# Kernel tuning notes

Hardware: AMD Instinct MI355X
Metric: run time of the kernel (lower is better)

Reference implementation:

```python
import jax, jax.numpy as jnp
import numpy as np
import math

B, CIN, COUT, NSC, H, W = 4, 3, 64, 3, 192, 192
HID = 64  # attention hidden channels


def setup_inputs() -> dict:
    key = jax.random.key(0)
    ks = jax.random.split(key, 10)
    pi = math.pi
    return {
        "x": jax.random.normal(ks[0], (B, CIN, H, W), jnp.float32),
        "freq": jax.random.uniform(ks[1], (NSC, COUT, CIN), jnp.float32) * pi,
        "theta": jax.random.uniform(ks[2], (NSC, COUT, CIN), jnp.float32) * pi,
        "sigma": jax.random.uniform(ks[3], (NSC, COUT, CIN), jnp.float32) * pi,
        "f0": jnp.ones((NSC, COUT, CIN), jnp.float32),
        "theta0": jnp.ones((NSC, COUT, CIN), jnp.float32),
        "attn_w1": jax.random.normal(ks[4], (HID, CIN), jnp.float32) / np.sqrt(CIN).astype(np.float32),
        "attn_b1": jnp.zeros((HID,), jnp.float32),
        "attn_w2": jax.random.normal(ks[5], (COUT * NSC, HID), jnp.float32) / np.sqrt(HID).astype(np.float32),
        "attn_b2": jnp.zeros((COUT * NSC,), jnp.float32),
        "bn_w": jnp.ones((COUT * NSC,), jnp.float32),
        "bn_b": jnp.zeros((COUT * NSC,), jnp.float32),
        "mixing_param": jax.random.uniform(ks[6], (1,), jnp.float32),
        "conv_w": jax.random.normal(ks[7], (COUT, CIN, 3, 3), jnp.float32) * 0.1,
        "freq_band_select": jax.random.uniform(ks[8], (COUT, CIN, 2), jnp.float32),
    }


def _forward(x, freq, theta, sigma, f0, theta0, attn_w1, attn_b1, attn_w2,
             attn_b2, bn_w, bn_b, mixing_param, conv_w, freq_band_select):
    b, cin, h, w = x.shape
    # torch.fft.fftshift default dim=None shifts ALL axes (incl. batch/channel)
    Xs = jnp.fft.fftshift(jnp.fft.fft2(x))  # [B,Cin,H,W] complex64

    # ---- multi-scale log-Gabor filter bank g[S,O,I,H,W] ----
    yy, xx = jnp.meshgrid(jnp.linspace(-1.0, 1.0, h), jnp.linspace(-1.0, 1.0, w), indexing="ij")
    r = jnp.sqrt(xx * xx + yy * yy + 1e-6)
    phi = jnp.arctan2(yy, xx)
    f0e = f0[..., None, None]
    sg = sigma[..., None, None]
    th = theta[..., None, None]
    th0 = theta0[..., None, None]
    fr = freq[..., None, None]
    log_gabor = jnp.exp(-(jnp.log(r) - jnp.log(f0e)) ** 2 / (2.0 * jnp.log(sg / f0e) ** 2))
    angular = jnp.exp(-(phi - th) ** 2 / (2.0 * th0 ** 2))
    g = log_gabor * angular * jnp.cos(fr * r) / (2.0 * math.pi * sg ** 2)  # [S,O,I,H,W]

    # ---- frequency attention: 1x1 conv -> ReLU -> 1x1 conv -> BN(train) -> softmax ----
    mag = jnp.abs(Xs)
    h1 = jax.nn.relu(jnp.einsum("oi,bihw->bohw", attn_w1, mag) + attn_b1[None, :, None, None])
    h2 = jnp.einsum("oi,bihw->bohw", attn_w2, h1) + attn_b2[None, :, None, None]
    mu = h2.mean(axis=(0, 2, 3))
    var = h2.var(axis=(0, 2, 3))  # biased, as torch BN training mode
    h2 = (h2 - mu[None, :, None, None]) * jax.lax.rsqrt(var + 1e-5)[None, :, None, None]
    h2 = h2 * bn_w[None, :, None, None] + bn_b[None, :, None, None]
    attn = jax.nn.softmax(h2, axis=1).reshape(b, NSC, COUT, h, w)  # view as [B,S,O,H,W]

    # ---- attention-weighted complex sum over (scale, out, in), then batch ----
    # attended_output(b) = sum_{s,o,i} attn[b,s,o]*g[s,o,i]*Xs[b,i]; torch then
    # sums over Cin and, via the [B,O,B,I,H,W] broadcast + sum(dims 2,3), over batch.
    Wr = jnp.einsum("bsohw,soihw->bihw", attn, g)  # real attention*filter weights
    A_tot = (Wr * Xs).sum(axis=(0, 1))             # [H,W] complex

    # ---- per-(out,in) frequency band mask (same index range on both axes) ----
    idx = jnp.floor((freq_band_select + 1.0) * 0.5 * h).astype(jnp.int32)  # [O,I,2]
    hr = jnp.arange(h)
    c = (hr[None, None, :] >= idx[..., 0:1]) & (hr[None, None, :] < idx[..., 1:2])  # [O,I,H]
    mask = (c[:, :, :, None] & c[:, :, None, :]).astype(jnp.float32)  # [O,I,H,W]
    Msum = mask.sum(axis=1)  # [O,H,W] (sum over Cin)

    # torch builds r[b0,o,b2,i,h,w]=A[b2]*M[o,i], ifftshift(all axes), ifft2,
    # real, sum over (b2,i). Rolls on summed axes commute with the sums, so this
    # equals ifftshift over (b0,o,h,w) of Q[b0,o]=A_tot*Msum[o] (const in b0).
    Q = jnp.broadcast_to((A_tot[None] * Msum.astype(Xs.dtype))[None], (b, COUT, h, w))
    xf = jnp.fft.ifft2(jnp.fft.ifftshift(Q)).real  # [B,O,H,W]

    xs = jax.lax.conv_general_dilated(
        x, conv_w, window_strides=(1, 1), padding=((1, 1), (1, 1)),
        dimension_numbers=("NCHW", "OIHW", "NCHW"))
    return mixing_param * xf + (1.0 - mixing_param) * xs


def reference(x, freq, theta, sigma, f0, theta0, attn_w1, attn_b1, attn_w2,
              attn_b2, bn_w, bn_b, mixing_param, conv_w, freq_band_select):
    return _forward(x, freq, theta, sigma, f0, theta0, attn_w1, attn_b1,
                    attn_w2, attn_b2, bn_w, bn_b, mixing_param, conv_w,
                    freq_band_select)
```

## Files before the change

### kernel.cpp

```cpp
#include <hip/hip_runtime.h>
#include <math.h>

#define NPIX  36864
#define PI2   6.28318530717958647692f

#define TW_OFF    0
#define PCA_OFF   1536
#define PCB_OFF   10752
#define W1F4_OFF  15360
#define W2B_OFF   16384
#define BN_OFF    65536
#define IDX_OFF   67072
#define M2_OFF    68608
#define T1_OFF    85248
#define XS_OFF    3624192
#define AH_OFF    7163136
#define XF_OFF    7458048
#define E2B_OFF   15846656
#define WS_FUSED  7458048
#define WS_SPLIT  16895232

#define PH_BYTES  14155776
#define E2C_OFF   14155776
#define OUT_MIN_ELEMS 9437184

typedef __attribute__((ext_vector_type(8))) short short8;
typedef __attribute__((ext_vector_type(4))) float floatx4;

__device__ __forceinline__ void bf16split(float v, unsigned short& hi, unsigned short& lo) {
    unsigned ub = __builtin_bit_cast(unsigned, v);
    hi = (unsigned short)(ub >> 16);
    float vh = __builtin_bit_cast(float, ub & 0xFFFF0000u);
    lo = (unsigned short)(__builtin_bit_cast(unsigned, v - vh) >> 16);
}

__global__ void k_pre(const float* freq, const float* theta, const float* sigma,
                      const float* f0, const float* theta0, const float* fbs,
                      const float* w1, const float* b1v, const float* w2,
                      char* ws, char* outw, int split) {
    float2* tw   = (float2*)(ws + TW_OFF);
    float4* pcA  = (float4*)(ws + PCA_OFF);
    float2* pcB  = (float2*)(ws + PCB_OFF);
    float4* w1f4 = (float4*)(ws + W1F4_OFF);
    unsigned short* w2b = (unsigned short*)(ws + W2B_OFF);
    int* idx = (int*)(ws + IDX_OFF);
    int gtid = blockIdx.x * blockDim.x + threadIdx.x;
    int gsz  = gridDim.x * blockDim.x;
    for (int n = gtid; n < 192; n += gsz) {
        float th = PI2 * (float)n / 192.0f;
        tw[n] = make_float2(cosf(th), sinf(th));
    }
    for (int t = gtid; t < 576; t += gsz) {
        int s = t / 192, rem = t % 192, o = rem / 3, i = rem % 3;
        float fr = freq[t], th = theta[t], sg = sigma[t], f0v = f0[t], th0 = theta0[t];
        float lg  = logf(sg / f0v);
        float a1  = -1.0f / (2.0f * lg * lg);
        float lf0 = logf(f0v);
        float a2  = -1.0f / (2.0f * th0 * th0);
        float lsc = -logf(PI2 * sg * sg);
        int pidx = (s*3 + i)*64 + o;
        pcA[pidx] = make_float4(a1, lf0, a2, th);
        pcB[pidx] = make_float2(fr, lsc);
    }
    for (int t = gtid; t < 64; t += gsz)
        w1f4[t] = make_float4(w1[t*3+0], w1[t*3+1], w1[t*3+2], b1v[t]);
    for (int u = gtid; u < 24576; u += gsz) {
        int j = u & 7;
        int l = (u >> 3) & 63;
        int hsel = (u >> 9) & 1;
        int rest = u >> 10;
        int kc = rest & 1;
        int t = rest >> 1;
        int k = kc*32 + (l>>4)*8 + j;
        int c = t*16 + (l & 15);
        float wv = w2[c*64 + k];
        unsigned short hi, lo;
        bf16split(wv, hi, lo);
        w2b[u] = hsel ? lo : hi;
    }
    for (int t = gtid; t < 192; t += gsz) {
        int lo = (int)floorf((fbs[t*2+0] + 1.0f) * 0.5f * 192.0f) - 96;
        int hi = (int)floorf((fbs[t*2+1] + 1.0f) * 0.5f * 192.0f) - 96;
        lo = max(0, min(96, lo));
        hi = max(0, min(96, hi));
        if (hi < lo) hi = lo;
        idx[t*2+0] = lo; idx[t*2+1] = hi;
    }
    if (split) {
        unsigned short* e2b = (unsigned short*)(ws + E2B_OFF);
        for (int u = gtid; u < 147456; u += gsz) {
            int j = u & 7;
            int l = (u >> 3) & 63;
            int half = (u >> 9) & 1;
            int rest = u >> 10;
            int kc = rest % 12, t = rest / 12;
            int k = kc*32 + ((l >> 4) << 3) + j;
            int w = k >> 1, comp = k & 1;
            int n = t*16 + (l & 15);
            int ang = (w * n) % 192;
            float th = PI2 * (float)ang / 192.0f;
            float v = comp ? sinf(th) : cosf(th);
            unsigned short hi, lo;
            bf16split(v, hi, lo);
            e2b[u] = half ? lo : hi;
        }
        unsigned short* e1 = (unsigned short*)(ws + T1_OFF);
        for (int u = gtid; u < 147456; u += gsz) {
            int j = u & 7;
            int l = (u >> 3) & 63;
            int half = (u >> 9) & 1;
            int rest = u >> 10;
            int kc = rest % 6;
            int comp = (rest / 6) & 1;
            int yt = rest / 12;
            int y = yt*16 + (l & 15);
            int h = kc*32 + ((l >> 4) << 3) + j;
            int ang = (h * y) % 192;
            float th = PI2 * (float)ang / 192.0f;
            float v = comp ? -sinf(th) : cosf(th);
            unsigned short hi, lo;
            bf16split(v, hi, lo);
            e1[u] = half ? lo : hi;
        }
        unsigned short* e2c = (unsigned short*)(outw + E2C_OFF);
        for (int u = gtid; u < 73728; u += gsz) {
            int j = u & 7;
            int l = (u >> 3) & 63;
            int half = (u >> 9) & 1;
            int rest = u >> 10;
            int kc = rest % 6, t = rest / 6;
            int k = kc*32 + ((l >> 4) << 3) + j;
            int w = k >> 1, comp = k & 1;
            int n = t*16 + (l & 15);
            int ang = (w * n) % 192;
            float th = PI2 * (float)ang / 192.0f;
            float v = comp ? sinf(th) : cosf(th);
            unsigned short hi, lo;
            bf16split(v, hi, lo);
            e2c[u] = half ? lo : hi;
        }
    }
}

__global__ __launch_bounds__(256) void k_dftm(const float* x, char* ws) {
    __shared__ __align__(16) float2 Ar[16][194];
    const unsigned short* e1  = (const unsigned short*)(ws + T1_OFF);
    const unsigned short* e2b = (const unsigned short*)(ws + E2B_OFF);
    float2* Xs = (float2*)(ws + XS_OFF);
    int tid = threadIdx.x;
    int bi = blockIdx.x / 12;
    int yt = blockIdx.x % 12;
    int y0 = yt * 16;
    int wave = tid >> 6, lane = tid & 63;
    int ml = lane & 15, qd = lane >> 4;
    const float* xp = x + bi * NPIX;
    union AB { short8 v; unsigned short u[8]; };
    floatx4 s1re[3], s1im[3];
#pragma unroll
    for (int tt = 0; tt < 3; tt++) {
        s1re[tt] = (floatx4){0.f,0.f,0.f,0.f};
        s1im[tt] = (floatx4){0.f,0.f,0.f,0.f};
    }
#pragma unroll 1
    for (int kc = 0; kc < 6; kc++) {
        const unsigned short* ac = e1 + (((((yt*2 + 0)*6 + kc)*2) << 9) + (lane << 3));
        const unsigned short* as = e1 + (((((yt*2 + 1)*6 + kc)*2) << 9) + (lane << 3));
        short8 ach = *(const short8*)ac;
        short8 acl = *(const short8*)(ac + 512);
        short8 ash = *(const short8*)as;
        short8 asl = *(const short8*)(as + 512);
#pragma unroll
        for (int tt = 0; tt < 3; tt++) {
            int nt = wave*3 + tt;
            AB bh8, bl8;
#pragma unroll
            for (int j = 0; j < 8; j++) {
                int h = kc*32 + qd*8 + j;
                float xv = xp[h*192 + nt*16 + ml];
                bf16split(xv, bh8.u[j], bl8.u[j]);
            }
            floatx4 r = s1re[tt];
            r = __builtin_amdgcn_mfma_f32_16x16x32_bf16(ach, bh8.v, r, 0, 0, 0);
            r = __builtin_amdgcn_mfma_f32_16x16x32_bf16(acl, bh8.v, r, 0, 0, 0);
            r = __builtin_amdgcn_mfma_f32_16x16x32_bf16(ach, bl8.v, r, 0, 0, 0);
            s1re[tt] = r;
            floatx4 q = s1im[tt];
            q = __builtin_amdgcn_mfma_f32_16x16x32_bf16(ash, bh8.v, q, 0, 0, 0);
            q = __builtin_amdgcn_mfma_f32_16x16x32_bf16(asl, bh8.v, q, 0, 0, 0);
            q = __builtin_amdgcn_mfma_f32_16x16x32_bf16(ash, bl8.v, q, 0, 0, 0);
            s1im[tt] = q;
        }
    }
#pragma unroll
    for (int tt = 0; tt < 3; tt++) {
        int w = (wave*3 + tt)*16 + ml;
#pragma unroll
        for (int r = 0; r < 4; r++)
            Ar[qd*4 + r][w] = make_float2(s1re[tt][r], s1im[tt][r]);
    }
    __syncthreads();
    floatx4 accre[3], accim[3];
#pragma unroll
    for (int tt = 0; tt < 3; tt++) {
        accre[tt] = (floatx4){0.f,0.f,0.f,0.f};
        accim[tt] = (floatx4){0.f,0.f,0.f,0.f};
    }
#pragma unroll 1
    for (int kc = 0; kc < 12; kc++) {
        int wb = kc*16 + qd*4;
        float4 p01 = *(const float4*)&Ar[ml][wb];
        float4 p23 = *(const float4*)&Ar[ml][wb + 2];
        float av[8]  = {p01.x, p01.y, p01.z, p01.w, p23.x, p23.y, p23.z, p23.w};
        float apv[8] = {p01.y, -p01.x, p01.w, -p01.z, p23.y, -p23.x, p23.w, -p23.z};
        AB ah, al, aph, apl;
#pragma unroll
        for (int j = 0; j < 8; j++) {
            bf16split(av[j],  ah.u[j],  al.u[j]);
            bf16split(apv[j], aph.u[j], apl.u[j]);
        }
#pragma unroll
        for (int tt = 0; tt < 3; tt++) {
            int t = wave*3 + tt;
            const unsigned short* bp = e2b + (((t*12 + kc)*2) << 9) + (lane << 3);
            short8 bh = *(const short8*)bp;
            short8 bl = *(const short8*)(bp + 512);
            floatx4 r = accre[tt];
            r = __builtin_amdgcn_mfma_f32_16x16x32_bf16(ah.v,  bh, r, 0, 0, 0);
            r = __builtin_amdgcn_mfma_f32_16x16x32_bf16(al.v,  bh, r, 0, 0, 0);
            r = __builtin_amdgcn_mfma_f32_16x16x32_bf16(ah.v,  bl, r, 0, 0, 0);
            accre[tt] = r;
            floatx4 q = accim[tt];
            q = __builtin_amdgcn_mfma_f32_16x16x32_bf16(aph.v, bh, q, 0, 0, 0);
            q = __builtin_amdgcn_mfma_f32_16x16x32_bf16(apl.v, bh, q, 0, 0, 0);
            q = __builtin_amdgcn_mfma_f32_16x16x32_bf16(aph.v, bl, q, 0, 0, 0);
            accim[tt] = q;
        }
    }
    int b = bi / 3, i = bi % 3;
    int bs = (b + 2) & 3;
    int is = (i + 1) % 3;
    float2* Xp = Xs + (bs*3 + is)*NPIX;
#pragma unroll
    for (int tt = 0; tt < 3; tt++) {
        int kx = (wave*3 + tt)*16 + ml;
        int ks = kx + 96; if (ks >= 192) ks -= 192;
#pragma unroll
        for (int r = 0; r < 4; r++) {
            int y = y0 + qd*4 + r;
            int ys = y + 96; if (ys >= 192) ys -= 192;
            Xp[ys*192 + ks] = make_float2(accre[tt][r], accim[tt][r]);
        }
    }
}

__global__ __launch_bounds__(192) void k_dft1(const float* x, char* ws) {
    __shared__ float2 twsh[192];
    const float2* tw = (const float2*)(ws + TW_OFF);
    float2* t1 = (float2*)(ws + T1_OFF);
    int tid = threadIdx.x;
    twsh[tid] = tw[tid];
    __syncthreads();
    int bi = blockIdx.x;
    int y0 = blockIdx.y * 4;
    int w  = tid;
    const float* xp = x + bi * NPIX;
    float2 acc[4];
#pragma unroll
    for (int d = 0; d < 4; d++) acc[d] = make_float2(0.f, 0.f);
    for (int h = 0; h < 192; h++) {
        float xv = xp[h*192 + w];
        int m = (h * y0) % 192;
#pragma unroll
        for (int d = 0; d < 4; d++) {
            float2 e = twsh[m];
            acc[d].x += xv * e.x;
            acc[d].y -= xv * e.y;
            m += h; if (m >= 192) m -= 192;
        }
    }
    float2* op = t1 + bi * NPIX;
#pragma unroll
    for (int d = 0; d < 4; d++) op[(y0 + d)*192 + w] = acc[d];
}

__global__ __launch_bounds__(192) void k_dft2(char* ws) {
    __shared__ float2 twsh[192];
    __shared__ float2 row[192];
    const float2* tw = (const float2*)(ws + TW_OFF);
    const float2* t1a = (const float2*)(ws + T1_OFF);
    float2* Xs = (float2*)(ws + XS_OFF);
    int tid = threadIdx.x;
    int bi = blockIdx.x, y = blockIdx.y;
    twsh[tid] = tw[tid];
    row[tid] = t1a[bi*NPIX + y*192 + tid];
    __syncthreads();
    int kx = tid;
    float2 st = twsh[kx];
    float2 acc = make_float2(0.f, 0.f);
#pragma unroll 1
    for (int w0 = 0; w0 < 192; w0 += 32) {
        float2 e = twsh[(w0 * kx) % 192];
#pragma unroll
        for (int w = 0; w < 32; w++) {
            float2 t = row[w0 + w];
            acc.x += t.x*e.x + t.y*e.y;
            acc.y += t.y*e.x - t.x*e.y;
            float ex = e.x*st.x - e.y*st.y;
            e.y = e.x*st.y + e.y*st.x;
            e.x = ex;
        }
    }
    int b = bi / 3, i = bi % 3;
    int bs = (b + 2) & 3;
    int is = (i + 1) % 3;
    int ys = y + 96;  if (ys >= 192) ys -= 192;
    int ks = kx + 96; if (ks >= 192) ks -= 192;
    Xs[(bs*3 + is)*NPIX + ys*192 + ks] = acc;
}

__global__ __launch_bounds__(256) void k_stats(char* ws) {
    __shared__ float magL[192];
    __shared__ float4 w1L[64];
    __shared__ float m1L[64];
    __shared__ __align__(16) unsigned short fragH[512*8];
    __shared__ __align__(16) unsigned short fragL[512*8];
    const float2* Xs = (const float2*)(ws + XS_OFF);
    float* M2 = (float*)(ws + M2_OFF);
    int tid = threadIdx.x;
    int wave = tid >> 6, lane = tid & 63;
    if (tid < 64) { w1L[tid] = ((const float4*)(ws + W1F4_OFF))[tid]; m1L[tid] = 0.f; }
    __syncthreads();
    int cch = wave*16 + (lane & 15);
    float4 wf = w1L[cch];
    float msum = 0.f;
    floatx4 acc[4];
#pragma unroll
    for (int nb = 0; nb < 4; nb++) acc[nb] = (floatx4){0.f, 0.f, 0.f, 0.f};
    union AB { short8 v; unsigned short u[8]; };
#pragma unroll 1
    for (int it = 0; it < 2; it++) {
        int tile = blockIdx.x * 2 + it;
        int S0 = tile * 64;
        int b = S0 / NPIX;
        int p0 = S0 - b*NPIX;
        if (tid < 192) {
            int i = tid >> 6, s = tid & 63;
            float2 v = Xs[(b*3 + i)*NPIX + p0 + s];
            magL[s*3 + i] = sqrtf(v.x*v.x + v.y*v.y);
        }
        __syncthreads();
#pragma unroll
        for (int kc = 0; kc < 2; kc++) {
            AB h8, l8;
#pragma unroll
            for (int j = 0; j < 8; j++) {
                int s = kc*32 + (lane>>4)*8 + j;
                float mg0 = magL[s*3], mg1 = magL[s*3+1], mg2 = magL[s*3+2];
                float hv = fmaxf(wf.w + wf.x*mg0 + wf.y*mg1 + wf.z*mg2, 0.f);
                msum += hv;
                bf16split(hv, h8.u[j], l8.u[j]);
            }
            int z = (kc*4 + wave)*64 + lane;
            *(short8*)&fragH[z*8] = h8.v;
            *(short8*)&fragL[z*8] = l8.v;
        }
        __syncthreads();
        short8 Ah0 = *(const short8*)&fragH[((0*4+wave)*64 + lane)*8];
        short8 Ah1 = *(const short8*)&fragH[((1*4+wave)*64 + lane)*8];
        short8 Al0 = *(const short8*)&fragL[((0*4+wave)*64 + lane)*8];
        short8 Al1 = *(const short8*)&fragL[((1*4+wave)*64 + lane)*8];
#pragma unroll
        for (int nb = 0; nb < 4; nb++) {
            short8 Bh0 = *(const short8*)&fragH[((0*4+nb)*64 + lane)*8];
            short8 Bh1 = *(const short8*)&fragH[((1*4+nb)*64 + lane)*8];
            short8 Bl0 = *(const short8*)&fragL[((0*4+nb)*64 + lane)*8];
            short8 Bl1 = *(const short8*)&fragL[((1*4+nb)*64 + lane)*8];
            floatx4 a = acc[nb];
            a = __builtin_amdgcn_mfma_f32_16x16x32_bf16(Ah0, Bh0, a, 0, 0, 0);
            a = __builtin_amdgcn_mfma_f32_16x16x32_bf16(Al0, Bh0, a, 0, 0, 0);
            a = __builtin_amdgcn_mfma_f32_16x16x32_bf16(Ah0, Bl0, a, 0, 0, 0);
            a = __builtin_amdgcn_mfma_f32_16x16x32_bf16(Ah1, Bh1, a, 0, 0, 0);
            a = __builtin_amdgcn_mfma_f32_16x16x32_bf16(Al1, Bh1, a, 0, 0, 0);
            a = __builtin_amdgcn_mfma_f32_16x16x32_bf16(Ah1, Bl1, a, 0, 0, 0);
            acc[nb] = a;
        }
        __syncthreads();
    }
#pragma unroll
    for (int nb = 0; nb < 4; nb++)
#pragma unroll
        for (int r = 0; r < 4; r++) {
            int row = wave*16 + (lane>>4)*4 + r;
            int col = nb*16 + (lane & 15);
            atomicAdd(&M2[row*64 + col], acc[nb][r]);
        }
    atomicAdd(&m1L[cch], msum);
    __syncthreads();
    if (tid < 64) atomicAdd(&M2[4096 + tid], m1L[tid]);
}

__global__ __launch_bounds__(64) void k_bn(const float* w2, const float* bnw,
                                           const float* bnb, char* ws) {
    const float* M2 = (const float*)(ws + M2_OFF);
    const float* m1 = M2 + 4096;
    float* bnsc = (float*)(ws + BN_OFF);
    float* bnsh = bnsc + 192;
    int c = blockIdx.x;
    int jj = threadIdx.x;
    const float* row = w2 + c*64;
    float rj = row[jj];
    float inner = 0.f;
    const float* m2r = M2 + jj*64;
    for (int k = 0; k < 64; k++) inner += row[k] * m2r[k];
    float qpart = rj * inner;
    float dpart = rj * m1[jj];
#pragma unroll
    for (int sh = 32; sh >= 1; sh >>= 1) {
        qpart += __shfl_xor(qpart, sh);
        dpart += __shfl_xor(dpart, sh);
    }
    if (jj == 0) {
        const float invN = 1.0f / 147456.0f;
        float d = dpart * invN;
        float qv = qpart * invN;
        float var = qv - d*d;
        float rstd = rsqrtf(var + 1e-5f);
        float scale = bnw[c] * rstd;
        bnsc[c] = scale;
        bnsh[c] = bnb[c] - d * scale;
    }
}

__global__ __launch_bounds__(256) void k_attn(char* ws) {
    __shared__ __align__(16) float4 pcAL[576];
    __shared__ float2 pcBL[576];
    __shared__ float4 w1L[64];
    const float2* Xs = (const float2*)(ws + XS_OFF);
    const float* bnA = (const float*)(ws + BN_OFF);
    const char* W2G = (const char*)(ws + W2B_OFF);
    float2* Ah = (float2*)(ws + AH_OFF);
    int tid = threadIdx.x;
    {
        const float4* pcA4 = (const float4*)(ws + PCA_OFF);
        const float2* pcB2 = (const float2*)(ws + PCB_OFF);
        for (int u = tid; u < 576; u += 256) {
            pcAL[u] = pcA4[u];
            pcBL[u] = pcB2[u];
        }
        if (tid < 64) w1L[tid] = ((const float4*)(ws + W1F4_OFF))[tid];
    }
    __syncthreads();
    int wave = tid >> 6, lane = tid & 63;
    int cl = lane & 15, q = lane >> 4;
    int g = blockIdx.x * 4 + wave;
    int pix0 = g * 4;

    union AB { short8 v; unsigned short u[8]; };
    int pb = pix0 + (cl >> 2), bb = cl & 3;
    float2 q0 = Xs[(bb*3+0)*NPIX + pb];
    float2 q1 = Xs[(bb*3+1)*NPIX + pb];
    float2 q2 = Xs[(bb*3+2)*NPIX + pb];
    float mg0 = sqrtf(q0.x*q0.x + q0.y*q0.y);
    float mg1 = sqrtf(q1.x*q1.x + q1.y*q1.y);
    float mg2 = sqrtf(q2.x*q2.x + q2.y*q2.y);
    AB ah[2], al[2];
#pragma unroll
    for (int kc = 0; kc < 2; kc++)
#pragma unroll
        for (int j = 0; j < 8; j++) {
            int k = kc*32 + q*8 + j;
            float4 wf = w1L[k];
            float hv = fmaxf(wf.w + wf.x*mg0 + wf.y*mg1 + wf.z*mg2, 0.f);
            bf16split(hv, ah[kc].u[j], al[kc].u[j]);
        }
    int pixE = pix0 + q;
    int hh = pixE / 192, ww = pixE - hh*192;
    float yy = -1.0f + (float)hh * (2.0f/191.0f);
    float xx = -1.0f + (float)ww * (2.0f/191.0f);
    float rr = sqrtf(xx*xx + yy*yy + 1e-6f);
    float lr = __logf(rr);
    float phi = atan2f(yy, xx);
    float sm0 = 0.f, sm1 = 0.f, sm2 = 0.f, sm3 = 0.f;
    float Wr[4][3];
#pragma unroll
    for (int r = 0; r < 4; r++) { Wr[r][0] = 0.f; Wr[r][1] = 0.f; Wr[r][2] = 0.f; }
#pragma unroll 2
    for (int t = 0; t < 12; t++) {
        floatx4 a = {0.f, 0.f, 0.f, 0.f};
#pragma unroll
        for (int kc = 0; kc < 2; kc++) {
            int ob = (((t*2 + kc)*2)*64 + lane)*16;
            short8 bh = *(const short8*)(W2G + ob);
            short8 bl = *(const short8*)(W2G + ob + 1024);
            a = __builtin_amdgcn_mfma_f32_16x16x32_bf16(ah[kc].v, bh, a, 0, 0, 0);
            a = __builtin_amdgcn_mfma_f32_16x16x32_bf16(al[kc].v, bh, a, 0, 0, 0);
            a = __builtin_amdgcn_mfma_f32_16x16x32_bf16(ah[kc].v, bl, a, 0, 0, 0);
        }
        int c = t*16 + cl;
        float sc_ = bnA[c], sh_ = bnA[192 + c];
        float e0 = __expf(a[0]*sc_ + sh_);
        float e1 = __expf(a[1]*sc_ + sh_);
        float e2 = __expf(a[2]*sc_ + sh_);
        float e3 = __expf(a[3]*sc_ + sh_);
        sm0 += e0; sm1 += e1; sm2 += e2; sm3 += e3;
        int sB = c >> 6, o = c & 63;
#pragma unroll
        for (int i = 0; i < 3; i++) {
            int pidx = (sB*3 + i)*64 + o;
            float4 pa = pcAL[pidx];
            float2 pbv = pcBL[pidx];
            float dl = lr - pa.y, dp = phi - pa.w;
            float gv = __expf(pa.x*dl*dl + pa.z*dp*dp + pbv.y) * __cosf(pbv.x*rr);
            Wr[0][i] += e0*gv; Wr[1][i] += e1*gv;
            Wr[2][i] += e2*gv; Wr[3][i] += e3*gv;
        }
    }
#pragma unroll
    for (int sh = 1; sh < 16; sh <<= 1) {
        sm0 += __shfl_xor(sm0, sh); sm1 += __shfl_xor(sm1, sh);
        sm2 += __shfl_xor(sm2, sh); sm3 += __shfl_xor(sm3, sh);
    }
    float inv0 = 1.0f/sm0, inv1 = 1.0f/sm1, inv2 = 1.0f/sm2, inv3 = 1.0f/sm3;
    float are = 0.f, aim = 0.f;
#pragma unroll
    for (int i = 0; i < 3; i++) {
        float2 x0 = Xs[(0*3+i)*NPIX + pixE];
        float2 x1 = Xs[(1*3+i)*NPIX + pixE];
        float2 x2 = Xs[(2*3+i)*NPIX + pixE];
        float2 x3 = Xs[(3*3+i)*NPIX + pixE];
        float w0v = Wr[0][i]*inv0, w1v = Wr[1][i]*inv1;
        float w2v = Wr[2][i]*inv2, w3v = Wr[3][i]*inv3;
        are += w0v*x0.x + w1v*x1.x + w2v*x2.x + w3v*x3.x;
        aim += w0v*x0.y + w1v*x1.y + w2v*x2.y + w3v*x3.y;
    }
#pragma unroll
    for (int sh = 1; sh < 16; sh <<= 1) {
        are += __shfl_xor(are, sh);
        aim += __shfl_xor(aim, sh);
    }
    if (cl == 0) {
        int hs = hh + 96; if (hs >= 192) hs -= 192;
        int wsx = ww + 96; if (wsx >= 192) wsx -= 192;
        Ah[hs*192 + wsx] = make_float2(are, aim);
    }
}

__global__ __launch_bounds__(192) void k_phpre(char* ws, char* outw) {
    __shared__ float2 AhL[96];
    const float2* tw  = (const float2*)(ws + TW_OFF);
    const float2* Ahp = (const float2*)(ws + AH_OFF);
    float2* Ph = (float2*)outw;
    int y = threadIdx.x;
    int w = blockIdx.x;
    if (y < 96) AhL[y] = Ahp[y*192 + w];
    __syncthreads();
    float2 step = tw[y];
    float ex = 1.f, ey = 0.f;
    float ax = 0.f, ay = 0.f;
    for (int h = 0; h < 96; h++) {
        float2 a = AhL[h];
        ax += a.x*ex - a.y*ey;
        ay += a.x*ey + a.y*ex;
        Ph[(h*96 + w)*192 + y] = make_float2(ax, ay);
        float t = ex*step.x - ey*step.y;
        ey = ex*step.y + ey*step.x;
        ex = t;
    }
}

__global__ __launch_bounds__(256) void k_ifftm(char* ws, char* outw) {
    __shared__ __align__(16) unsigned short AhiL[16*200];
    __shared__ __align__(16) unsigned short AloL[16*200];
    __shared__ int iL[3], iH[3];
    const float2* Ph = (const float2*)outw;
    const unsigned short* e2c = (const unsigned short*)(outw + E2C_OFF);
    const int* idx = (const int*)(ws + IDX_OFF);
    float* xf = (float*)(ws + XF_OFF);
    int tid = threadIdx.x;
    int o  = blockIdx.x / 12;
    int ys = blockIdx.x % 12;
    int op = (o + 32) & 63;
    if (tid < 3) { iL[tid] = idx[(op*3 + tid)*2]; iH[tid] = idx[(op*3 + tid)*2 + 1]; }
    __syncthreads();
    for (int u = tid; u < 1536; u += 256) {
        int w = u >> 4, yy = u & 15;
        int y = ys*16 + yy;
        float sr = 0.f, si = 0.f;
#pragma unroll
        for (int i = 0; i < 3; i++) {
            int lo = iL[i], hi = iH[i];
            if (w >= lo && w < hi) {
                float2 a = Ph[((hi-1)*96 + w)*192 + y];
                sr += a.x; si += a.y;
                if (lo > 0) {
                    float2 b2 = Ph[((lo-1)*96 + w)*192 + y];
                    sr -= b2.x; si -= b2.y;
                }
            }
        }
        unsigned short rh, rl, ih, il;
        bf16split(sr, rh, rl);
        bf16split(-si, ih, il);
        *(unsigned*)&AhiL[yy*200 + 2*w] = (unsigned)rh | ((unsigned)ih << 16);
        *(unsigned*)&AloL[yy*200 + 2*w] = (unsigned)rl | ((unsigned)il << 16);
    }
    __syncthreads();
    int wave = tid >> 6, lane = tid & 63;
    int ml = lane & 15, qd = lane >> 4;
    const float s = 1.0f / 36864.0f;
#pragma unroll 1
    for (int ntl = 0; ntl < 3; ntl++) {
        int nt = wave*3 + ntl;
        floatx4 acc = (floatx4){0.f,0.f,0.f,0.f};
#pragma unroll
        for (int kc = 0; kc < 6; kc++) {
            const unsigned short* bp = e2c + ((nt*6 + kc) << 10) + (lane << 3);
            short8 bh = *(const short8*)bp;
            short8 bl = *(const short8*)(bp + 512);
            int ka = kc*32 + qd*8;
            short8 ah = *(const short8*)&AhiL[ml*200 + ka];
            short8 al = *(const short8*)&AloL[ml*200 + ka];
            acc = __builtin_amdgcn_mfma_f32_16x16x32_bf16(ah, bh, acc, 0, 0, 0);
            acc = __builtin_amdgcn_mfma_f32_16x16x32_bf16(al, bh, acc, 0, 0, 0);
            acc = __builtin_amdgcn_mfma_f32_16x16x32_bf16(ah, bl, acc, 0, 0, 0);
        }
#pragma unroll
        for (int r = 0; r < 4; r++) {
            int y = ys*16 + qd*4 + r;
            int x = nt*16 + ml;
            xf[o*NPIX + y*192 + x] = acc[r] * s;
        }
    }
}

__global__ __launch_bounds__(192) void k_conv(const float* x, const float* convw,
                                              const float* mixp, const float* xf,
                                              float* out) {
    int col = threadIdx.x;
    int y = blockIdx.x;
    int b = blockIdx.y;
    int o0 = blockIdx.z * 16;
    float xv[27];
#pragma unroll
    for (int i = 0; i < 3; i++)
#pragma unroll
        for (int dy = 0; dy < 3; dy++)
#pragma unroll
            for (int dx = 0; dx < 3; dx++) {
                int yq = y + dy - 1, xq = col + dx - 1;
                bool ok = (yq >= 0) & (yq < 192) & (xq >= 0) & (xq < 192);
                xv[(i*3 + dy)*3 + dx] = ok ? x[(b*3+i)*NPIX + yq*192 + xq] : 0.f;
            }
    float mixv = mixp[0];
    float onem = 1.0f - mixv;
    for (int o = o0; o < o0 + 16; o++) {
        float s = 0.f;
#pragma unroll
        for (int c = 0; c < 27; c++) s += xv[c] * convw[o*27 + c];
        float xfv = xf[o*NPIX + y*192 + col];
        out[((b*64 + o)*192 + y)*192 + col] = mixv*xfv + onem*s;
    }
}

__global__ __launch_bounds__(192) void k_final(const float* x, const float* convw,
                                               const float* mixp, float* out, char* ws) {
    __shared__ float2 twsh[192];
    __shared__ float2 Ssh[3][96];
    __shared__ float cwsh[27];
    __shared__ int iL[3], iH[3];
    const float2* tw = (const float2*)(ws + TW_OFF);
    const int* idx = (const int*)(ws + IDX_OFF);
    const float2* Ah = (const float2*)(ws + AH_OFF);
    int tid = threadIdx.x;
    int y = blockIdx.x;
    int o = blockIdx.y;
    int op = (o + 32) & 63;
    twsh[tid] = tw[tid];
    if (tid < 27) cwsh[tid] = convw[o*27 + tid];
    if (tid < 3) { iL[tid] = idx[(op*3 + tid)*2]; iH[tid] = idx[(op*3 + tid)*2 + 1]; }
    __syncthreads();
    int l0 = iL[0], u0 = iH[0], l1 = iL[1], u1 = iH[1], l2 = iL[2], u2 = iH[2];
    int n0 = u0 - l0, n1 = u1 - l1, n2 = u2 - l2;
    int p1 = n0 + n1, T = p1 + n2;
    for (int t = tid; t < T; t += 192) {
        int i, off, lo, hi;
        if (t < n0)      { i = 0; off = t;      lo = l0; hi = u0; }
        else if (t < p1) { i = 1; off = t - n0; lo = l1; hi = u1; }
        else             { i = 2; off = t - p1; lo = l2; hi = u2; }
        int wq = lo + off;
        float sx = 0.f, sy = 0.f;
        int m = (lo * y) % 192;
        for (int hq = lo; hq < hi; hq++) {
            float2 a = Ah[hq*192 + wq];
            float2 e = twsh[m];
            sx += a.x*e.x - a.y*e.y;
            sy += a.x*e.y + a.y*e.x;
            m += y; if (m >= 192) m -= 192;
        }
        Ssh[i][off] = make_float2(sx, sy);
    }
    __syncthreads();
    int col = tid;
    float accre = 0.f;
#pragma unroll
    for (int i = 0; i < 3; i++) {
        int lo = iL[i];
        int wi = iH[i] - lo;
        int m = (lo * col) % 192;
        for (int off = 0; off < wi; off++) {
            float2 S = Ssh[i][off];
            float2 e = twsh[m];
            accre += S.x*e.x - S.y*e.y;
            m += col; if (m >= 192) m -= 192;
        }
    }
    float xfv = accre * (1.0f / 36864.0f);
    float mixv = mixp[0];
    float onem = 1.0f - mixv;
#pragma unroll
    for (int b = 0; b < 4; b++) {
        float s = 0.f;
#pragma unroll
        for (int i = 0; i < 3; i++) {
            const float* xp = x + (b*3 + i)*NPIX;
#pragma unroll
            for (int dy = -1; dy <= 1; dy++) {
                int yq = y + dy;
                if (yq < 0 || yq >= 192) continue;
                const float* rowp = xp + yq*192;
#pragma unroll
                for (int dx = -1; dx <= 1; dx++) {
                    int xq = col + dx;
                    if (xq < 0 || xq >= 192) continue;
                    s += rowp[xq] * cwsh[i*9 + (dy+1)*3 + (dx+1)];
                }
            }
        }
        out[((b*64 + o)*192 + y)*192 + col] = mixv*xfv + onem*s;
    }
}

extern "C" void kernel_launch(void* const* d_in, const int* in_sizes, int n_in,
                              void* d_out, int out_size, void* d_ws, size_t ws_size,
                              hipStream_t stream) {
    const float* x      = (const float*)d_in[0];
    const float* freq   = (const float*)d_in[1];
    const float* theta  = (const float*)d_in[2];
    const float* sigma  = (const float*)d_in[3];
    const float* f0     = (const float*)d_in[4];
    const float* theta0 = (const float*)d_in[5];
    const float* aw1    = (const float*)d_in[6];
    const float* ab1    = (const float*)d_in[7];
    const float* aw2    = (const float*)d_in[8];
    const float* bnw    = (const float*)d_in[10];
    const float* bnb    = (const float*)d_in[11];
    const float* mixp   = (const float*)d_in[12];
    const float* convw  = (const float*)d_in[13];
    const float* fbs    = (const float*)d_in[14];
    float* out = (float*)d_out;
    char* ws = (char*)d_ws;
    char* outc = (char*)d_out;
    if (ws_size < (size_t)WS_FUSED) return;
    int split = (ws_size >= (size_t)WS_SPLIT) && (out_size >= OUT_MIN_ELEMS);

    hipMemsetAsync(ws + M2_OFF, 0, 16640, stream);
    k_pre  <<<192, 256, 0, stream>>>(freq, theta, sigma, f0, theta0, fbs,
                                     aw1, ab1, aw2, ws, outc, split);
    if (split) {
        k_dftm <<<144, 256, 0, stream>>>(x, ws);
    } else {
        k_dft1 <<<dim3(12, 48), 192, 0, stream>>>(x, ws);
        k_dft2 <<<dim3(12, 192), 192, 0, stream>>>(ws);
    }
    k_stats<<<1152, 256, 0, stream>>>(ws);
    k_bn   <<<192, 64, 0, stream>>>(aw2, bnw, bnb, ws);
    k_attn <<<2304, 256, 0, stream>>>(ws);
    if (split) {
        k_phpre<<<96, 192, 0, stream>>>(ws, outc);
        k_ifftm<<<768, 256, 0, stream>>>(ws, outc);
        k_conv <<<dim3(192, 4, 4), 192, 0, stream>>>(x, convw, mixp,
                                                     (const float*)(ws + XF_OFF), out);
    } else {
        k_final<<<dim3(192, 64), 192, 0, stream>>>(x, convw, mixp, out, ws);
    }
}
```

Baseline: 242.8 us.

## Split fused MFMA DFT into K-split first pass and separate second-pass kernel

The fused two-stage DFT kernel (144 blocks) is split into two kernels. The first pass now splits the reduction dimension in half across 288 blocks and writes partial results to two workspace halves. The second kernel sums the halves into shared memory and does the column DFT. This is meant to raise parallelism on the many-CU GPU, at the cost of an extra kernel launch and a global round trip for the intermediate.

```diff
diff --git a/kernel.cpp b/kernel.cpp
--- a/kernel.cpp
+++ b/kernel.cpp
@@ -16,6 +16,7 @@
 #define XS_OFF    3624192
 #define AH_OFF    7163136
 #define XF_OFF    7458048
+#define T1B_HALF  3538944
 #define E2B_OFF   15846656
 #define WS_FUSED  7458048
 #define WS_SPLIT  16895232
@@ -142,14 +143,13 @@
     }
 }
 
-__global__ __launch_bounds__(256) void k_dftm(const float* x, char* ws) {
-    __shared__ __align__(16) float2 Ar[16][194];
-    const unsigned short* e1  = (const unsigned short*)(ws + T1_OFF);
-    const unsigned short* e2b = (const unsigned short*)(ws + E2B_OFF);
-    float2* Xs = (float2*)(ws + XS_OFF);
+__global__ __launch_bounds__(256) void k_dft1m(const float* x, char* ws) {
+    const unsigned short* e1 = (const unsigned short*)(ws + T1_OFF);
     int tid = threadIdx.x;
-    int bi = blockIdx.x / 12;
-    int yt = blockIdx.x % 12;
+    int b = blockIdx.x;
+    int z  = b & 1;
+    int yt = (b >> 1) % 12;
+    int bi = b / 24;
     int y0 = yt * 16;
     int wave = tid >> 6, lane = tid & 63;
     int ml = lane & 15, qd = lane >> 4;
@@ -162,7 +162,8 @@
         s1im[tt] = (floatx4){0.f,0.f,0.f,0.f};
     }
 #pragma unroll 1
-    for (int kc = 0; kc < 6; kc++) {
+    for (int kq = 0; kq < 3; kq++) {
+        int kc = z*3 + kq;
         const unsigned short* ac = e1 + (((((yt*2 + 0)*6 + kc)*2) << 9) + (lane << 3));
         const unsigned short* as = e1 + (((((yt*2 + 1)*6 + kc)*2) << 9) + (lane << 3));
         short8 ach = *(const short8*)ac;
@@ -191,20 +192,42 @@
             s1im[tt] = q;
         }
     }
+    float2* op = (float2*)(ws + XF_OFF + (size_t)z * T1B_HALF) + bi * NPIX;
 #pragma unroll
     for (int tt = 0; tt < 3; tt++) {
         int w = (wave*3 + tt)*16 + ml;
 #pragma unroll
         for (int r = 0; r < 4; r++)
-            Ar[qd*4 + r][w] = make_float2(s1re[tt][r], s1im[tt][r]);
-    }
-    __syncthreads();
+            op[(y0 + qd*4 + r)*192 + w] = make_float2(s1re[tt][r], s1im[tt][r]);
+    }
+}
+
+__global__ __launch_bounds__(256) void k_dft2m(char* ws) {
+    __shared__ __align__(16) float2 Ar[16][194];
+    const float2* t1a = (const float2*)(ws + XF_OFF);
+    const float2* t1b = (const float2*)(ws + XF_OFF + T1B_HALF);
+    const unsigned short* e2b = (const unsigned short*)(ws + E2B_OFF);
+    float2* Xs = (float2*)(ws + XS_OFF);
+    int tid = threadIdx.x;
+    int bi = blockIdx.x / 12;
+    int y0 = (blockIdx.x % 12) * 16;
+    for (int u = tid; u < 3072; u += 256) {
+        int m = u / 192, w = u - m*192;
+        float2 v = t1a[bi*NPIX + (y0+m)*192 + w];
+        float2 v2 = t1b[bi*NPIX + (y0+m)*192 + w];
+        v.x += v2.x; v.y += v2.y;
+        Ar[m][w] = v;
+    }
+    __syncthreads();
+    int wave = tid >> 6, lane = tid & 63;
+    int ml = lane & 15, qd = lane >> 4;
     floatx4 accre[3], accim[3];
 #pragma unroll
     for (int tt = 0; tt < 3; tt++) {
         accre[tt] = (floatx4){0.f,0.f,0.f,0.f};
         accim[tt] = (floatx4){0.f,0.f,0.f,0.f};
     }
+    union AB { short8 v; unsigned short u[8]; };
 #pragma unroll 1
     for (int kc = 0; kc < 12; kc++) {
         int wb = kc*16 + qd*4;
@@ -767,7 +790,8 @@
     k_pre  <<<192, 256, 0, stream>>>(freq, theta, sigma, f0, theta0, fbs,
                                      aw1, ab1, aw2, ws, outc, split);
     if (split) {
-        k_dftm <<<144, 256, 0, stream>>>(x, ws);
+        k_dft1m<<<288, 256, 0, stream>>>(x, ws);
+        k_dft2m<<<144, 256, 0, stream>>>(ws);
     } else {
         k_dft1 <<<dim3(12, 48), 192, 0, stream>>>(x, ws);
         k_dft2 <<<dim3(12, 192), 192, 0, stream>>>(ws);
```

After: 246.8 us. About the same (+1.7%).
